# Kernel optimization log

Hardware: AMD Instinct MI355X
Metric: run time of the kernel (lower is better)

The kernel has to match this reference:

```python
import jax, jax.numpy as jnp
import numpy as np

MAXDISP = 192


def setup_inputs() -> dict:
    key = jax.random.key(0)
    x = jax.random.normal(key, (2, 1, 48, 64, 128), dtype=jnp.float32)
    return {"x": x}


def reference(x):
    B, C, D, H, W = x.shape  # C == 1, low-res cost volume
    # Trilinear upsample, align_corners=False (half-pixel centers) ==
    # jax.image.resize method='linear'. Target: [B,1,maxdisp+1, 4H, 4W].
    vol = jax.image.resize(x, (B, C, MAXDISP + 1, H * 4, W * 4), method="linear")
    vol = vol[:, 0]  # squeeze channel -> [B, D', H', W']
    # Softmin over disparity = softmax(-vol, axis=1)
    probs = jax.nn.softmax(-vol, axis=1)
    disp = jnp.arange(MAXDISP + 1, dtype=probs.dtype)
    out = jnp.einsum("bdhw,d->bhw", probs, disp)  # [B, 4H, 4W]
    return out
```

## Files before the change

### kernel.cpp

```cpp
#include <hip/hip_runtime.h>

#define D_IN  48
#define H_IN  64
#define W_IN  128
#define D_OUT 193
#define H_OUT 256
#define W_OUT 512
#define NCOL  34

typedef float f32x2 __attribute__((ext_vector_type(2)));


__device__ __forceinline__ float exp2_fast(float x) {
#if __has_builtin(__builtin_amdgcn_exp2f)
    return __builtin_amdgcn_exp2f(x);
#else
    float r;
    asm("v_exp_f32 %0, %1" : "=v"(r) : "v"(x));
    return r;
#endif
}

template<int Q>
__device__ __forceinline__ void compute_quarter2(const float* baseA, const float* baseB,
                                                 float fwA, float fwB,
                                                 f32x2& s_out, f32x2& ds_out) {
    constexpr int K0   = (Q == 0) ? 0  : (Q == 1) ? 11 : (Q == 2) ? 23  : 35;
    constexpr int KHI  = (Q == 0) ? 11 : (Q == 1) ? 23 : (Q == 2) ? 35  : 46;
    constexpr int DMIN = (Q == 0) ? 2  : (Q == 1) ? 49 : (Q == 2) ? 97  : 145;
    constexpr int DMAX = (Q == 0) ? 48 : (Q == 1) ? 96 : (Q == 2) ? 144 : 190;

    const float* pA = baseA + K0 * NCOL;
    const float* pB = baseB + K0 * NCOL;
    f32x2 g = { fmaf(fwA, pA[1] - pA[0], pA[0]),
                fmaf(fwB, pB[1] - pB[0], pB[0]) };

    f32x2 s = {0.f, 0.f}, ds = {0.f, 0.f};

    if (Q == 0) {
        f32x2 e = { exp2_fast(g.x), exp2_fast(g.y) };
        s = e + e;
        ds = e;
    }

    #pragma unroll
    for (int k = K0; k <= KHI; ++k) {
        const float* qA = baseA + (k + 1) * NCOL;
        const float* qB = baseB + (k + 1) * NCOL;
        f32x2 gn = { fmaf(fwA, qA[1] - qA[0], qA[0]),
                     fmaf(fwB, qB[1] - qB[0], qB[0]) };
        f32x2 delta = gn - g;
        int dlo = (386 * k + 240) / 96;           if (dlo < DMIN) dlo = DMIN;
        int dhi = (386 * (k + 1) + 240) / 96 - 1; if (dhi > DMAX) dhi = DMAX;
        #pragma unroll
        for (int d = dlo; d <= dhi; ++d) {
            float f = (float)(96 * d - 145 - 386 * k) * (1.0f / 386.0f);
            f32x2 fv = {f, f};
            f32x2 arg = __builtin_elementwise_fma(fv, delta, g);
            f32x2 e = { exp2_fast(arg.x), exp2_fast(arg.y) };
            s = s + e;
            f32x2 dv = {(float)d, (float)d};
            ds = __builtin_elementwise_fma(dv, e, ds);
        }
        g = gn;
    }

    if (Q == 3) {
        f32x2 e = { exp2_fast(g.x), exp2_fast(g.y) };
        s = s + e + e;
        f32x2 c383 = {383.f, 383.f};
        ds = __builtin_elementwise_fma(c383, e, ds);
    }

    s_out = s;
    ds_out = ds;
}

__global__ __launch_bounds__(256) void disp_kernel(const float* __restrict__ x,
                                                   float* __restrict__ out) {
    __shared__ float sm[D_IN * NCOL];
    __shared__ f32x2 red_s[256], red_d[256];

    int t = threadIdx.x;
    int slot = t & 63;
    int qq = t >> 6;
    int p0 = blockIdx.x << 7;
    int pA = p0 + 2 * slot;
    int wA = pA & (W_OUT - 1);
    int wB = wA + 1;
    int h = (pA >> 9) & (H_OUT - 1);
    int b = pA >> 17;
    int wblk = p0 & (W_OUT - 1);

    float hf = (h + 0.5f) * 0.25f - 0.5f;
    float hfl = floorf(hf);
    int h0 = (int)hfl;
    float fh = hf - hfl;
    int hp; float fhp;
    if (h0 < 0)              { hp = 0;        fhp = 0.f; }
    else if (h0 >= H_IN - 1) { hp = H_IN - 2; fhp = 1.f; }
    else                     { hp = h0;       fhp = fh;  }

    auto winterp = [](int w, int& wp, float& fwp) {
        float wf = (w + 0.5f) * 0.25f - 0.5f;
        float wfl = floorf(wf);
        int w0 = (int)wfl;
        float fw = wf - wfl;
        if (w0 < 0)              { wp = 0;        fwp = 0.f; }
        else if (w0 >= W_IN - 1) { wp = W_IN - 2; fwp = 1.f; }
        else                     { wp = w0;       fwp = fw;  }
    };
    int wpA, wpB; float fwA, fwB;
    winterp(wA, wpA, fwA);
    winterp(wB, wpB, fwB);

    const float L2E = 1.4426950408889634f;
    int col0 = (wblk >> 2) - 1; if (col0 < 0) col0 = 0;
    const float* xrow = x + (size_t)b * (D_IN * H_IN * W_IN) + hp * W_IN;
    float fhn = -L2E * fhp;
    for (int idx = t; idx < D_IN * NCOL; idx += 256) {
        int k = idx / NCOL;
        int j = idx - k * NCOL;
        int col = col0 + j; if (col > W_IN - 1) col = W_IN - 1;
        const float* q = xrow + k * (H_IN * W_IN) + col;
        float a = q[0], bq = q[W_IN];
        sm[idx] = fmaf(fhn, bq - a, a * (-L2E));
    }
    __syncthreads();

    const float* baseA = &sm[wpA - col0];
    const float* baseB = &sm[wpB - col0];
    f32x2 S, D;
    if      (qq == 0) compute_quarter2<0>(baseA, baseB, fwA, fwB, S, D);
    else if (qq == 1) compute_quarter2<1>(baseA, baseB, fwA, fwB, S, D);
    else if (qq == 2) compute_quarter2<2>(baseA, baseB, fwA, fwB, S, D);
    else              compute_quarter2<3>(baseA, baseB, fwA, fwB, S, D);

    red_s[t] = S; red_d[t] = D;
    __syncthreads();

    if (t < 64) {
        f32x2 den = (red_s[t] + red_s[t + 64]) + (red_s[t + 128] + red_s[t + 192]);
        f32x2 num = (red_d[t] + red_d[t + 64]) + (red_d[t + 128] + red_d[t + 192]);
        int p = p0 + 2 * t;
#if __has_builtin(__builtin_amdgcn_rcpf)
        out[p]     = num.x * __builtin_amdgcn_rcpf(den.x);
        out[p + 1] = num.y * __builtin_amdgcn_rcpf(den.y);
#else
        out[p]     = num.x / den.x;
        out[p + 1] = num.y / den.y;
#endif
    }
}

extern "C" void kernel_launch(void* const* d_in, const int* in_sizes, int n_in,
                              void* d_out, int out_size, void* d_ws, size_t ws_size,
                              hipStream_t stream) {
    const float* x = (const float*)d_in[0];
    float* out = (float*)d_out;
    int total_pixels = 2 * H_OUT * W_OUT;
    int blocks = total_pixels / 128;
    disp_kernel<<<blocks, 256, 0, stream>>>(x, out);
}
```

Measured before the change: 15.58 us.

## Replace per-sample exp2 with geometric recurrence and share column pair for two pixels

Inside each low-res depth segment the exponent is linear in d, so the change computes one exp2 at the first sample plus one ratio exp2 and gets the remaining terms by repeated multiplication, removing most transcendental calls. The paired output pixels always fall in the same source column pair, so their weights are now closed-form constants and shared LDS loads replace the separate per-pixel lookups. The staging loop also replaces the per-element div/mod by NCOL with incremental index updates. The multiplicative chain can accumulate rounding error over up to five steps per segment.

```diff
diff --git a/kernel.cpp b/kernel.cpp
--- a/kernel.cpp
+++ b/kernel.cpp
@@ -22,18 +22,17 @@
 }
 
 template<int Q>
-__device__ __forceinline__ void compute_quarter2(const float* baseA, const float* baseB,
-                                                 float fwA, float fwB,
+__device__ __forceinline__ void compute_quarter2(const float* base, f32x2 fw2,
                                                  f32x2& s_out, f32x2& ds_out) {
     constexpr int K0   = (Q == 0) ? 0  : (Q == 1) ? 11 : (Q == 2) ? 23  : 35;
     constexpr int KHI  = (Q == 0) ? 11 : (Q == 1) ? 23 : (Q == 2) ? 35  : 46;
     constexpr int DMIN = (Q == 0) ? 2  : (Q == 1) ? 49 : (Q == 2) ? 97  : 145;
     constexpr int DMAX = (Q == 0) ? 48 : (Q == 1) ? 96 : (Q == 2) ? 144 : 190;
 
-    const float* pA = baseA + K0 * NCOL;
-    const float* pB = baseB + K0 * NCOL;
-    f32x2 g = { fmaf(fwA, pA[1] - pA[0], pA[0]),
-                fmaf(fwB, pB[1] - pB[0], pB[0]) };
+    const float* pr = base + K0 * NCOL;
+    float a0 = pr[0], b0 = pr[1];
+    f32x2 g = __builtin_elementwise_fma(fw2, (f32x2){b0 - a0, b0 - a0},
+                                        (f32x2){a0, a0});
 
     f32x2 s = {0.f, 0.f}, ds = {0.f, 0.f};
 
@@ -45,22 +44,26 @@
 
     #pragma unroll
     for (int k = K0; k <= KHI; ++k) {
-        const float* qA = baseA + (k + 1) * NCOL;
-        const float* qB = baseB + (k + 1) * NCOL;
-        f32x2 gn = { fmaf(fwA, qA[1] - qA[0], qA[0]),
-                     fmaf(fwB, qB[1] - qB[0], qB[0]) };
+        const float* pn = base + (k + 1) * NCOL;
+        float an = pn[0], bn = pn[1];
+        f32x2 gn = __builtin_elementwise_fma(fw2, (f32x2){bn - an, bn - an},
+                                             (f32x2){an, an});
         f32x2 delta = gn - g;
         int dlo = (386 * k + 240) / 96;           if (dlo < DMIN) dlo = DMIN;
         int dhi = (386 * (k + 1) + 240) / 96 - 1; if (dhi > DMAX) dhi = DMAX;
+
+        float f0 = (float)(96 * dlo - 145 - 386 * k) * (1.0f / 386.0f);
+        f32x2 arg0 = __builtin_elementwise_fma((f32x2){f0, f0}, delta, g);
+        f32x2 e = { exp2_fast(arg0.x), exp2_fast(arg0.y) };
+        f32x2 rarg = delta * (96.0f / 386.0f);
+        f32x2 r = { exp2_fast(rarg.x), exp2_fast(rarg.y) };
+
         #pragma unroll
         for (int d = dlo; d <= dhi; ++d) {
-            float f = (float)(96 * d - 145 - 386 * k) * (1.0f / 386.0f);
-            f32x2 fv = {f, f};
-            f32x2 arg = __builtin_elementwise_fma(fv, delta, g);
-            f32x2 e = { exp2_fast(arg.x), exp2_fast(arg.y) };
             s = s + e;
             f32x2 dv = {(float)d, (float)d};
             ds = __builtin_elementwise_fma(dv, e, ds);
+            if (d != dhi) e = e * r;
         }
         g = gn;
     }
@@ -68,8 +71,7 @@
     if (Q == 3) {
         f32x2 e = { exp2_fast(g.x), exp2_fast(g.y) };
         s = s + e + e;
-        f32x2 c383 = {383.f, 383.f};
-        ds = __builtin_elementwise_fma(c383, e, ds);
+        ds = __builtin_elementwise_fma((f32x2){383.f, 383.f}, e, ds);
     }
 
     s_out = s;
@@ -87,7 +89,6 @@
     int p0 = blockIdx.x << 7;
     int pA = p0 + 2 * slot;
     int wA = pA & (W_OUT - 1);
-    int wB = wA + 1;
     int h = (pA >> 9) & (H_OUT - 1);
     int b = pA >> 17;
     int wblk = p0 & (W_OUT - 1);
@@ -101,40 +102,38 @@
     else if (h0 >= H_IN - 1) { hp = H_IN - 2; fhp = 1.f; }
     else                     { hp = h0;       fhp = fh;  }
 
-    auto winterp = [](int w, int& wp, float& fwp) {
-        float wf = (w + 0.5f) * 0.25f - 0.5f;
-        float wfl = floorf(wf);
-        int w0 = (int)wfl;
-        float fw = wf - wfl;
-        if (w0 < 0)              { wp = 0;        fwp = 0.f; }
-        else if (w0 >= W_IN - 1) { wp = W_IN - 2; fwp = 1.f; }
-        else                     { wp = w0;       fwp = fw;  }
-    };
-    int wpA, wpB; float fwA, fwB;
-    winterp(wA, wpA, fwA);
-    winterp(wB, wpB, fwB);
+    int wp; float fA, fB;
+    if (wA == 0)              { wp = 0;              fA = 0.f;    fB = 0.f;    }
+    else if (wA == W_OUT - 2) { wp = W_IN - 2;       fA = 1.f;    fB = 1.f;    }
+    else if (wA & 2)          { wp = wA >> 2;        fA = 0.125f; fB = 0.375f; }
+    else                      { wp = (wA >> 2) - 1;  fA = 0.625f; fB = 0.875f; }
+    f32x2 fw2 = {fA, fB};
 
     const float L2E = 1.4426950408889634f;
     int col0 = (wblk >> 2) - 1; if (col0 < 0) col0 = 0;
     const float* xrow = x + (size_t)b * (D_IN * H_IN * W_IN) + hp * W_IN;
     float fhn = -L2E * fhp;
-    for (int idx = t; idx < D_IN * NCOL; idx += 256) {
-        int k = idx / NCOL;
-        int j = idx - k * NCOL;
-        int col = col0 + j; if (col > W_IN - 1) col = W_IN - 1;
-        const float* q = xrow + k * (H_IN * W_IN) + col;
-        float a = q[0], bq = q[W_IN];
-        sm[idx] = fmaf(fhn, bq - a, a * (-L2E));
+    {
+        int j = t % NCOL;
+        int k = t / NCOL;
+        for (int idx = t; idx < D_IN * NCOL; idx += 256) {
+            int col = col0 + j; if (col > W_IN - 1) col = W_IN - 1;
+            const float* q = xrow + k * (H_IN * W_IN) + col;
+            float a = q[0], bq = q[W_IN];
+            sm[idx] = fmaf(fhn, bq - a, a * (-L2E));
+            j += 256 - 7 * NCOL;
+            k += 7;
+            if (j >= NCOL) { j -= NCOL; k += 1; }
+        }
     }
     __syncthreads();
 
-    const float* baseA = &sm[wpA - col0];
-    const float* baseB = &sm[wpB - col0];
+    const float* base = &sm[wp - col0];
     f32x2 S, D;
-    if      (qq == 0) compute_quarter2<0>(baseA, baseB, fwA, fwB, S, D);
-    else if (qq == 1) compute_quarter2<1>(baseA, baseB, fwA, fwB, S, D);
-    else if (qq == 2) compute_quarter2<2>(baseA, baseB, fwA, fwB, S, D);
-    else              compute_quarter2<3>(baseA, baseB, fwA, fwB, S, D);
+    if      (qq == 0) compute_quarter2<0>(base, fw2, S, D);
+    else if (qq == 1) compute_quarter2<1>(base, fw2, S, D);
+    else if (qq == 2) compute_quarter2<2>(base, fw2, S, D);
+    else              compute_quarter2<3>(base, fw2, S, D);
 
     red_s[t] = S; red_d[t] = D;
     __syncthreads();
```

Result: faster. 13.38 us (-14.1%).
